# Optimization experiments

Hardware: AMD Instinct MI355X
Metric: run time of the kernel (lower is better)

The kernel has to match this reference:

```python
import jax, jax.numpy as jnp
import numpy as np


def setup_inputs() -> dict:
    key = jax.random.key(0)
    ks = jax.random.split(key, 13)
    HID = 256
    N = 2 * HID                      # hidden_dim * 2
    B_DOC, S, T_K = 32, 40, 64      # docs, sentences/doc, max words/sentence
    B_SENT = B_DOC * S               # total sentences = sum(sent_lens)
    MAX_DOC_LEN = S * T_K
    f = jnp.float32
    sc = jnp.float32(0.05)
    sent_lens = jnp.full((B_DOC,), S, dtype=jnp.int32)
    inp = {
        "s_t_hat": jax.random.normal(ks[0], (B_DOC, N), f),
        "encoder_outputs": jax.random.normal(ks[1], (B_SENT, T_K, N), f),
        "encoder_feature": jax.random.normal(ks[2], (B_SENT * T_K, N), f) * jnp.float32(0.5),
        "seq_lens2": jax.random.randint(ks[3], (B_SENT,), T_K // 2, T_K + 1, dtype=jnp.int32),
        "sent_s_t_hat": jax.random.normal(ks[4], (B_DOC, N), f),
        "sent_enc_outputs": jax.random.normal(ks[5], (B_DOC, S, N), f),
        "sent_enc_feature": jax.random.normal(ks[6], (B_DOC * S, N), f) * jnp.float32(0.5),
        "sent_enc_padding_mask": (jnp.arange(S)[None, :] < sent_lens[:, None]).astype(f),
        "sent_lens": sent_lens,
        "max_doc_len": MAX_DOC_LEN,
        "coverage": jnp.zeros((B_SENT, T_K), f),
        "Wd": jax.random.normal(ks[7], (N, N), f) * sc,
        "bd": jax.random.normal(ks[8], (N,), f) * sc,
        "v_w": jax.random.normal(ks[9], (N,), f) * sc,
        "Wsd": jax.random.normal(ks[10], (N, N), f) * sc,
        "bsd": jax.random.normal(ks[11], (N,), f) * sc,
        "sv_w": jax.random.normal(ks[12], (N,), f) * sc,
    }
    return inp


def _excl_cumsum(x):
    return jnp.cumsum(x) - x


def reference(s_t_hat, encoder_outputs, encoder_feature, seq_lens2, sent_s_t_hat,
              sent_enc_outputs, sent_enc_feature, sent_enc_padding_mask, sent_lens,
              max_doc_len, coverage, Wd, bd, v_w, Wsd, bsd, sv_w):
    B_SENT, T_K, N = encoder_outputs.shape
    B_DOC, S, _ = sent_enc_outputs.shape
    dtype = encoder_outputs.dtype

    # sentence s -> owning doc (replaces first Python loop: broadcast dec_fea per doc)
    doc_ids = jnp.repeat(jnp.arange(B_DOC), sent_lens, total_repeat_length=B_SENT)

    # ---- word-level additive attention over each sentence ----
    dec_fea = s_t_hat @ Wd + bd                              # [B_DOC, N]
    att = jnp.tanh(encoder_feature.reshape(B_SENT, T_K, N) + dec_fea[doc_ids][:, None, :])
    scores = att @ v_w                                        # [B_SENT, T_K]
    w_mask = (jnp.arange(T_K)[None, :] < seq_lens2[:, None]).astype(dtype)
    w_attn_ = jax.nn.softmax(scores, axis=1) * w_mask
    w_attn = w_attn_ / w_attn_.sum(1, keepdims=True)          # [B_SENT, T_K]

    # ---- sentence-level additive attention over each doc ----
    sent_dec_fea = sent_s_t_hat @ Wsd + bsd                   # [B_DOC, N]
    sent_att = jnp.tanh(sent_enc_feature.reshape(B_DOC, S, N) + sent_dec_fea[:, None, :])
    sent_scores = sent_att @ sv_w                             # [B_DOC, S]
    sent_attn_ = jax.nn.softmax(sent_scores, axis=1) * sent_enc_padding_mask
    sent_attn_dist = sent_attn_ / sent_attn_.sum(1, keepdims=True)

    # ---- ragged flatten: scatter valid words of each sentence into its doc stream ----
    sent_start = _excl_cumsum(sent_lens)                      # first sentence idx per doc
    sent_local = jnp.arange(B_SENT) - sent_start[doc_ids]     # sentence pos within doc
    mult_attn = sent_attn_dist[doc_ids, sent_local][:, None] * w_attn  # [B_SENT, T_K]

    word_cum = _excl_cumsum(seq_lens2)                        # global word offsets
    doc_word_off = word_cum - word_cum[sent_start[doc_ids]]   # offset within doc
    pos = doc_word_off[:, None] + jnp.arange(T_K)[None, :]    # [B_SENT, T_K]
    valid = jnp.arange(T_K)[None, :] < seq_lens2[:, None]
    flat = jnp.where(valid, doc_ids[:, None] * max_doc_len + pos, B_DOC * max_doc_len)
    flat = flat.reshape(-1)

    enc_output2 = (jnp.zeros((B_DOC * max_doc_len, N), dtype)
                   .at[flat].set(encoder_outputs.reshape(-1, N), mode="drop")
                   .reshape(B_DOC, max_doc_len, N))
    attn_dist_sw = (jnp.zeros((B_DOC * max_doc_len,), dtype)
                    .at[flat].set(mult_attn.reshape(-1), mode="drop")
                    .reshape(B_DOC, max_doc_len))

    c_t = jnp.einsum("bl,bln->bn", attn_dist_sw, enc_output2)  # [B_DOC, N]
    return (c_t, attn_dist_sw, coverage, sent_attn_dist)
```

## Files before the change

### kernel.cpp

```cpp
#include <hip/hip_runtime.h>
#include <hip/hip_bf16.h>
#include <math.h>

#define B_DOC 32
#define S_MAX 40
#define T_K 64
#define N_DIM 512
#define B_SENT (B_DOC * S_MAX)
#define MAXDOC (S_MAX * T_K)
#define KCHUNK 4

__device__ __forceinline__ float fast_tanh(float x) {
    float e = __expf(2.0f * x);
    return 1.0f - 2.0f * __builtin_amdgcn_rcpf(e + 1.0f);
}

__global__ __launch_bounds__(256) void prep_kernel(
        const int* __restrict__ seq_lens2, const int* __restrict__ sent_lens,
        int* __restrict__ doc_ids, int* __restrict__ sent_local,
        int* __restrict__ doc_word_off, int* __restrict__ sent_start_g,
        int* __restrict__ doc_words_total) {
    __shared__ int ss[B_DOC + 1];
    __shared__ int wc[B_SENT + 1];
    __shared__ int wsum[4];
    int tid = threadIdx.x;
    int lane = tid & 63, w = tid >> 6;

    int ls[5];
    #pragma unroll
    for (int k = 0; k < 5; ++k) ls[k] = seq_lens2[tid * 5 + k];
    int sum = ls[0] + ls[1] + ls[2] + ls[3] + ls[4];

    int scan = sum;
    #pragma unroll
    for (int off = 1; off < 64; off <<= 1) {
        int v = __shfl_up(scan, off, 64);
        if (lane >= off) scan += v;
    }
    if (lane == 63) wsum[w] = scan;

    if (w == 0) {
        int sl = (lane < B_DOC) ? sent_lens[lane] : 0;
        int sc2 = sl;
        #pragma unroll
        for (int off = 1; off < 64; off <<= 1) {
            int v = __shfl_up(sc2, off, 64);
            if (lane >= off) sc2 += v;
        }
        if (lane < B_DOC) ss[lane + 1] = sc2;
        if (lane == 0) ss[0] = 0;
    }
    __syncthreads();

    int wbase = 0;
    for (int i = 0; i < w; ++i) wbase += wsum[i];
    int excl = wbase + scan - sum;
    #pragma unroll
    for (int k = 0; k < 5; ++k) { wc[tid * 5 + k] = excl; excl += ls[k]; }
    if (tid == 255) wc[B_SENT] = excl;
    __syncthreads();

    if (tid <= B_DOC) sent_start_g[tid] = ss[tid];
    if (tid < B_DOC) doc_words_total[tid] = wc[ss[tid + 1]] - wc[ss[tid]];

    for (int i = tid; i < B_SENT; i += 256) {
        int lo = 0, hi = B_DOC - 1;
        while (lo < hi) { int mid = (lo + hi + 1) >> 1; if (ss[mid] <= i) lo = mid; else hi = mid - 1; }
        doc_ids[i] = lo;
        sent_local[i] = i - ss[lo];
        doc_word_off[i] = wc[i] - wc[ss[lo]];
    }
}

__global__ __launch_bounds__(256) void fea_kernel(
        const float* __restrict__ s_t_hat, const float* __restrict__ sent_s_t_hat,
        const float* __restrict__ Wd, const float* __restrict__ bd,
        const float* __restrict__ Wsd, const float* __restrict__ bsd,
        float* __restrict__ fea_part) {
    int blk = blockIdx.x;
    int c = blk & (KCHUNK - 1);
    int b = (blk >> 2) & 31;
    int m = blk >> 7;
    const int KC = N_DIM / KCHUNK;
    const float* x = (m ? sent_s_t_hat : s_t_hat) + b * N_DIM + c * KC;
    const float* W = (m ? Wsd : Wd) + (size_t)c * KC * N_DIM;
    const float* bias = (m ? bsd : bd);
    float* out = fea_part + ((size_t)(m * 32 + b) * KCHUNK + c) * N_DIM;
    __shared__ float xs[128];
    int tid = threadIdx.x;
    if (tid < KC) xs[tid] = x[tid];
    __syncthreads();
    float a0 = 0.f, a1 = 0.f;
    if (c == 0) { a0 = bias[tid]; a1 = bias[tid + 256]; }
    #pragma unroll 8
    for (int k = 0; k < KC; ++k) {
        float xv = xs[k];
        a0 = fmaf(xv, W[k * N_DIM + tid], a0);
        a1 = fmaf(xv, W[k * N_DIM + tid + 256], a1);
    }
    out[tid] = a0;
    out[tid + 256] = a1;
}

__global__ __launch_bounds__(256) void sent_attn_kernel(
        const float* __restrict__ sef, const float* __restrict__ fea_part,
        const float* __restrict__ sv_w, const float* __restrict__ mask,
        float* __restrict__ out_sent) {
    int b = blockIdx.x;
    __shared__ float df[N_DIM];
    __shared__ float vw[N_DIM];
    __shared__ float sc[S_MAX];
    int tid = threadIdx.x;
    const float* fp = fea_part + (size_t)(32 + b) * KCHUNK * N_DIM;
    for (int i = tid; i < N_DIM; i += 256) {
        df[i] = fp[i] + fp[N_DIM + i] + fp[2 * N_DIM + i] + fp[3 * N_DIM + i];
        vw[i] = sv_w[i];
    }
    __syncthreads();
    int w = tid >> 6, lane = tid & 63;
    const float4* sef4 = (const float4*)(sef + (size_t)b * S_MAX * N_DIM);
    const float4* df4 = (const float4*)df;
    const float4* vw4 = (const float4*)vw;
    for (int t = w; t < S_MAX; t += 4) {
        float acc = 0.0f;
        #pragma unroll
        for (int j = 0; j < 2; ++j) {
            int n4 = lane + 64 * j;
            float4 e = sef4[t * 128 + n4];
            float4 d = df4[n4];
            float4 v = vw4[n4];
            acc = fmaf(v.x, fast_tanh(e.x + d.x), acc);
            acc = fmaf(v.y, fast_tanh(e.y + d.y), acc);
            acc = fmaf(v.z, fast_tanh(e.z + d.z), acc);
            acc = fmaf(v.w, fast_tanh(e.w + d.w), acc);
        }
        #pragma unroll
        for (int off = 32; off >= 1; off >>= 1) acc += __shfl_xor(acc, off, 64);
        if (lane == 0) sc[t] = acc;
    }
    __syncthreads();
    if (tid < 64) {
        bool valid = tid < S_MAX;
        float x = valid ? sc[tid] : -INFINITY;
        float m = x;
        #pragma unroll
        for (int off = 32; off >= 1; off >>= 1) m = fmaxf(m, __shfl_xor(m, off, 64));
        float mk = valid ? mask[b * S_MAX + tid] : 0.0f;
        float e = valid ? __expf(x - m) * mk : 0.0f;
        float ssum = e;
        #pragma unroll
        for (int off = 32; off >= 1; off >>= 1) ssum += __shfl_xor(ssum, off, 64);
        if (valid) out_sent[b * S_MAX + tid] = e / ssum;
    }
}

__global__ __launch_bounds__(256) void fused_kernel(
        const float* __restrict__ ef, const float* __restrict__ eo,
        const float* __restrict__ fea_part, const float* __restrict__ v_w,
        const float* __restrict__ sent_attn, const int* __restrict__ seq_lens2,
        const int* __restrict__ doc_ids, const int* __restrict__ sent_local,
        const int* __restrict__ doc_word_off, const int* __restrict__ sent_start,
        const int* __restrict__ doc_words_total, const int* __restrict__ mdl,
        const float* __restrict__ cov_in,
        float* __restrict__ part, float* __restrict__ out_attn,
        float* __restrict__ out_cov) {
    int s = blockIdx.x;
    int tid = threadIdx.x;
    __shared__ float df[N_DIM];
    __shared__ float vw[N_DIM];
    __shared__ float sc[T_K];
    __shared__ float mult[T_K];
    __shared__ float4 red[256];

    int doc = doc_ids[s];
    int len = seq_lens2[s];
    int maxdoc = mdl[0];

    const float* fp = fea_part + (size_t)doc * KCHUNK * N_DIM;
    for (int i = tid; i < N_DIM; i += 256) {
        df[i] = fp[i] + fp[N_DIM + i] + fp[2 * N_DIM + i] + fp[3 * N_DIM + i];
        vw[i] = v_w[i];
    }
    if (tid < T_K) out_cov[s * T_K + tid] = cov_in[s * T_K + tid];
    __syncthreads();

    int w = tid >> 6, lane = tid & 63;
    const float4* ef4 = (const float4*)(ef + (size_t)s * T_K * N_DIM);
    const float4* df4 = (const float4*)df;
    const float4* vw4 = (const float4*)vw;
    for (int t = w; t < len; t += 4) {
        float acc = 0.0f;
        #pragma unroll
        for (int j = 0; j < 2; ++j) {
            int n4 = lane + 64 * j;
            float4 e = ef4[t * 128 + n4];
            float4 d = df4[n4];
            float4 v = vw4[n4];
            acc = fmaf(v.x, fast_tanh(e.x + d.x), acc);
            acc = fmaf(v.y, fast_tanh(e.y + d.y), acc);
            acc = fmaf(v.z, fast_tanh(e.z + d.z), acc);
            acc = fmaf(v.w, fast_tanh(e.w + d.w), acc);
        }
        #pragma unroll
        for (int off = 32; off >= 1; off >>= 1) acc += __shfl_xor(acc, off, 64);
        if (lane == 0) sc[t] = acc;
    }
    __syncthreads();
    if (tid < T_K) {
        bool valid = tid < len;
        float x = valid ? sc[tid] : -INFINITY;
        float m = x;
        #pragma unroll
        for (int off = 32; off >= 1; off >>= 1) m = fmaxf(m, __shfl_xor(m, off, 64));
        float e = valid ? __expf(x - m) : 0.0f;
        float ssum = e;
        #pragma unroll
        for (int off = 32; off >= 1; off >>= 1) ssum += __shfl_xor(ssum, off, 64);
        float sa = sent_attn[doc * S_MAX + sent_local[s]];
        float mu = valid ? sa * (e / ssum) : 0.0f;
        mult[tid] = mu;
        if (valid) out_attn[(size_t)doc * maxdoc + doc_word_off[s] + tid] = mu;
    }
    if (s + 1 == sent_start[doc + 1]) {
        int dwt = doc_words_total[doc];
        for (int i = dwt + tid; i < maxdoc; i += 256)
            out_attn[(size_t)doc * maxdoc + i] = 0.0f;
    }
    __syncthreads();

    int nq = tid & 127;
    int tq = tid >> 7;
    float4 acc = {0.f, 0.f, 0.f, 0.f};
    const float4* e4 = (const float4*)(eo + (size_t)s * T_K * N_DIM);
    for (int t = tq; t < len; t += 2) {
        float m = mult[t];
        float4 e = e4[t * 128 + nq];
        acc.x = fmaf(m, e.x, acc.x);
        acc.y = fmaf(m, e.y, acc.y);
        acc.z = fmaf(m, e.z, acc.z);
        acc.w = fmaf(m, e.w, acc.w);
    }
    red[tid] = acc;
    __syncthreads();
    if (tq == 0) {
        float4 a = red[nq];
        float4 o = red[nq + 128];
        float4 r = {a.x + o.x, a.y + o.y, a.z + o.z, a.w + o.w};
        ((float4*)(part + (size_t)s * N_DIM))[nq] = r;
    }
}

__global__ __launch_bounds__(128) void reduce_kernel(
        const float* __restrict__ part, const int* __restrict__ sent_start,
        float* __restrict__ c_t) {
    int b = blockIdx.x;
    int nq = threadIdx.x;
    int st = sent_start[b], en = sent_start[b + 1];
    float4 acc = {0.f, 0.f, 0.f, 0.f};
    for (int s = st; s < en; ++s) {
        float4 p = ((const float4*)(part + (size_t)s * N_DIM))[nq];
        acc.x += p.x; acc.y += p.y; acc.z += p.z; acc.w += p.w;
    }
    ((float4*)(c_t + (size_t)b * N_DIM))[nq] = acc;
}

extern "C" void kernel_launch(void* const* d_in, const int* in_sizes, int n_in,
                              void* d_out, int out_size, void* d_ws, size_t ws_size,
                              hipStream_t stream) {
    const float* s_t_hat        = (const float*)d_in[0];
    const float* encoder_out    = (const float*)d_in[1];
    const float* encoder_feat   = (const float*)d_in[2];
    const int*   seq_lens2      = (const int*)d_in[3];
    const float* sent_s_t_hat   = (const float*)d_in[4];
    const float* sent_enc_feat  = (const float*)d_in[6];
    const float* sent_pad_mask  = (const float*)d_in[7];
    const int*   sent_lens      = (const int*)d_in[8];
    const int*   max_doc_len    = (const int*)d_in[9];
    const float* coverage       = (const float*)d_in[10];
    const float* Wd             = (const float*)d_in[11];
    const float* bd             = (const float*)d_in[12];
    const float* v_w            = (const float*)d_in[13];
    const float* Wsd            = (const float*)d_in[14];
    const float* bsd            = (const float*)d_in[15];
    const float* sv_w           = (const float*)d_in[16];

    float* out      = (float*)d_out;
    float* o_ct     = out;
    float* o_attn   = out + B_DOC * N_DIM;
    float* o_cov    = o_attn + B_DOC * MAXDOC;
    float* o_sent   = o_cov + B_SENT * T_K;

    float* ws          = (float*)d_ws;
    float* fea_part    = ws;
    float* part        = ws + 131072;
    int*   ints        = (int*)(ws + 131072 + 655360);
    int*   doc_ids     = ints;
    int*   sent_local  = ints + B_SENT;
    int*   doc_w_off   = ints + 2 * B_SENT;
    int*   sent_start  = ints + 3 * B_SENT;
    int*   doc_wtot    = ints + 3 * B_SENT + 33;

    prep_kernel<<<1, 256, 0, stream>>>(seq_lens2, sent_lens, doc_ids, sent_local,
                                       doc_w_off, sent_start, doc_wtot);
    fea_kernel<<<2 * 32 * KCHUNK, 256, 0, stream>>>(s_t_hat, sent_s_t_hat, Wd, bd,
                                                    Wsd, bsd, fea_part);
    sent_attn_kernel<<<B_DOC, 256, 0, stream>>>(sent_enc_feat, fea_part, sv_w,
                                                sent_pad_mask, o_sent);
    fused_kernel<<<B_SENT, 256, 0, stream>>>(encoder_feat, encoder_out, fea_part,
                                             v_w, o_sent, seq_lens2, doc_ids,
                                             sent_local, doc_w_off, sent_start,
                                             doc_wtot, max_doc_len, coverage,
                                             part, o_attn, o_cov);
    reduce_kernel<<<B_DOC, 128, 0, stream>>>(part, sent_start, o_ct);
}
```

Measured before the change: 80.51 us.

## Fuse word attention with context accumulation via online softmax; merge prep and fea kernels

The word-level scoring and the weighted sum over encoder outputs now run in a single pass. Each wavefront keeps a running max, a running sum and a rescaled accumulator, and the four wavefronts are merged at the end. This removes the separate softmax phase, the extra barriers and the second loop over encoder_outputs, and it prefetches the next encoder_feature row. The prep and feature-projection kernels are merged into one launch, with one extra block handling the scans, which saves a kernel launch. The cost is more registers and extra exp/rescale work per step.

```diff
diff --git a/kernel.cpp b/kernel.cpp
--- a/kernel.cpp
+++ b/kernel.cpp
@@ -15,91 +15,90 @@
     return 1.0f - 2.0f * __builtin_amdgcn_rcpf(e + 1.0f);
 }
 
-__global__ __launch_bounds__(256) void prep_kernel(
+__global__ __launch_bounds__(256) void prep_fea_kernel(
         const int* __restrict__ seq_lens2, const int* __restrict__ sent_lens,
+        const float* __restrict__ s_t_hat, const float* __restrict__ sent_s_t_hat,
+        const float* __restrict__ Wd, const float* __restrict__ bd,
+        const float* __restrict__ Wsd, const float* __restrict__ bsd,
+        float* __restrict__ fea_part,
         int* __restrict__ doc_ids, int* __restrict__ sent_local,
         int* __restrict__ doc_word_off, int* __restrict__ sent_start_g,
         int* __restrict__ doc_words_total) {
-    __shared__ int ss[B_DOC + 1];
-    __shared__ int wc[B_SENT + 1];
-    __shared__ int wsum[4];
     int tid = threadIdx.x;
-    int lane = tid & 63, w = tid >> 6;
-
-    int ls[5];
-    #pragma unroll
-    for (int k = 0; k < 5; ++k) ls[k] = seq_lens2[tid * 5 + k];
-    int sum = ls[0] + ls[1] + ls[2] + ls[3] + ls[4];
-
-    int scan = sum;
-    #pragma unroll
-    for (int off = 1; off < 64; off <<= 1) {
-        int v = __shfl_up(scan, off, 64);
-        if (lane >= off) scan += v;
-    }
-    if (lane == 63) wsum[w] = scan;
-
-    if (w == 0) {
-        int sl = (lane < B_DOC) ? sent_lens[lane] : 0;
-        int sc2 = sl;
+    if (blockIdx.x == 256) {
+        __shared__ int ss[B_DOC + 1];
+        __shared__ int wc[B_SENT + 1];
+        __shared__ int wsum[4];
+        int lane = tid & 63, w = tid >> 6;
+
+        int ls[5];
+        #pragma unroll
+        for (int k = 0; k < 5; ++k) ls[k] = seq_lens2[tid * 5 + k];
+        int sum = ls[0] + ls[1] + ls[2] + ls[3] + ls[4];
+
+        int scan = sum;
         #pragma unroll
         for (int off = 1; off < 64; off <<= 1) {
-            int v = __shfl_up(sc2, off, 64);
-            if (lane >= off) sc2 += v;
-        }
-        if (lane < B_DOC) ss[lane + 1] = sc2;
-        if (lane == 0) ss[0] = 0;
-    }
-    __syncthreads();
-
-    int wbase = 0;
-    for (int i = 0; i < w; ++i) wbase += wsum[i];
-    int excl = wbase + scan - sum;
-    #pragma unroll
-    for (int k = 0; k < 5; ++k) { wc[tid * 5 + k] = excl; excl += ls[k]; }
-    if (tid == 255) wc[B_SENT] = excl;
-    __syncthreads();
-
-    if (tid <= B_DOC) sent_start_g[tid] = ss[tid];
-    if (tid < B_DOC) doc_words_total[tid] = wc[ss[tid + 1]] - wc[ss[tid]];
-
-    for (int i = tid; i < B_SENT; i += 256) {
-        int lo = 0, hi = B_DOC - 1;
-        while (lo < hi) { int mid = (lo + hi + 1) >> 1; if (ss[mid] <= i) lo = mid; else hi = mid - 1; }
-        doc_ids[i] = lo;
-        sent_local[i] = i - ss[lo];
-        doc_word_off[i] = wc[i] - wc[ss[lo]];
-    }
-}
-
-__global__ __launch_bounds__(256) void fea_kernel(
-        const float* __restrict__ s_t_hat, const float* __restrict__ sent_s_t_hat,
-        const float* __restrict__ Wd, const float* __restrict__ bd,
-        const float* __restrict__ Wsd, const float* __restrict__ bsd,
-        float* __restrict__ fea_part) {
-    int blk = blockIdx.x;
-    int c = blk & (KCHUNK - 1);
-    int b = (blk >> 2) & 31;
-    int m = blk >> 7;
-    const int KC = N_DIM / KCHUNK;
-    const float* x = (m ? sent_s_t_hat : s_t_hat) + b * N_DIM + c * KC;
-    const float* W = (m ? Wsd : Wd) + (size_t)c * KC * N_DIM;
-    const float* bias = (m ? bsd : bd);
-    float* out = fea_part + ((size_t)(m * 32 + b) * KCHUNK + c) * N_DIM;
-    __shared__ float xs[128];
-    int tid = threadIdx.x;
-    if (tid < KC) xs[tid] = x[tid];
-    __syncthreads();
-    float a0 = 0.f, a1 = 0.f;
-    if (c == 0) { a0 = bias[tid]; a1 = bias[tid + 256]; }
-    #pragma unroll 8
-    for (int k = 0; k < KC; ++k) {
-        float xv = xs[k];
-        a0 = fmaf(xv, W[k * N_DIM + tid], a0);
-        a1 = fmaf(xv, W[k * N_DIM + tid + 256], a1);
-    }
-    out[tid] = a0;
-    out[tid + 256] = a1;
+            int v = __shfl_up(scan, off, 64);
+            if (lane >= off) scan += v;
+        }
+        if (lane == 63) wsum[w] = scan;
+
+        if (w == 0) {
+            int sl = (lane < B_DOC) ? sent_lens[lane] : 0;
+            int sc2 = sl;
+            #pragma unroll
+            for (int off = 1; off < 64; off <<= 1) {
+                int v = __shfl_up(sc2, off, 64);
+                if (lane >= off) sc2 += v;
+            }
+            if (lane < B_DOC) ss[lane + 1] = sc2;
+            if (lane == 0) ss[0] = 0;
+        }
+        __syncthreads();
+
+        int wbase = 0;
+        for (int i = 0; i < w; ++i) wbase += wsum[i];
+        int excl = wbase + scan - sum;
+        #pragma unroll
+        for (int k = 0; k < 5; ++k) { wc[tid * 5 + k] = excl; excl += ls[k]; }
+        if (tid == 255) wc[B_SENT] = excl;
+        __syncthreads();
+
+        if (tid <= B_DOC) sent_start_g[tid] = ss[tid];
+        if (tid < B_DOC) doc_words_total[tid] = wc[ss[tid + 1]] - wc[ss[tid]];
+
+        for (int i = tid; i < B_SENT; i += 256) {
+            int lo = 0, hi = B_DOC - 1;
+            while (lo < hi) { int mid = (lo + hi + 1) >> 1; if (ss[mid] <= i) lo = mid; else hi = mid - 1; }
+            doc_ids[i] = lo;
+            sent_local[i] = i - ss[lo];
+            doc_word_off[i] = wc[i] - wc[ss[lo]];
+        }
+    } else {
+        int blk = blockIdx.x;
+        int c = blk & (KCHUNK - 1);
+        int b = (blk >> 2) & 31;
+        int m = blk >> 7;
+        const int KC = N_DIM / KCHUNK;
+        const float* x = (m ? sent_s_t_hat : s_t_hat) + b * N_DIM + c * KC;
+        const float* W = (m ? Wsd : Wd) + (size_t)c * KC * N_DIM;
+        const float* bias = (m ? bsd : bd);
+        float* out = fea_part + ((size_t)(m * 32 + b) * KCHUNK + c) * N_DIM;
+        __shared__ float xs[128];
+        if (tid < KC) xs[tid] = x[tid];
+        __syncthreads();
+        float a0 = 0.f, a1 = 0.f;
+        if (c == 0) { a0 = bias[tid]; a1 = bias[tid + 256]; }
+        #pragma unroll 8
+        for (int k = 0; k < KC; ++k) {
+            float xv = xs[k];
+            a0 = fmaf(xv, W[k * N_DIM + tid], a0);
+            a1 = fmaf(xv, W[k * N_DIM + tid + 256], a1);
+        }
+        out[tid] = a0;
+        out[tid + 256] = a1;
+    }
 }
 
 __global__ __launch_bounds__(256) void sent_attn_kernel(
@@ -154,7 +153,7 @@
     }
 }
 
-__global__ __launch_bounds__(256) void fused_kernel(
+__global__ __launch_bounds__(256, 4) void fused_kernel(
         const float* __restrict__ ef, const float* __restrict__ eo,
         const float* __restrict__ fea_part, const float* __restrict__ v_w,
         const float* __restrict__ sent_attn, const int* __restrict__ seq_lens2,
@@ -166,87 +165,97 @@
         float* __restrict__ out_cov) {
     int s = blockIdx.x;
     int tid = threadIdx.x;
-    __shared__ float df[N_DIM];
-    __shared__ float vw[N_DIM];
+    int w = tid >> 6, lane = tid & 63;
     __shared__ float sc[T_K];
-    __shared__ float mult[T_K];
-    __shared__ float4 red[256];
+    __shared__ float wm[4], wl[4];
+    __shared__ float4 red[4][128];
 
     int doc = doc_ids[s];
     int len = seq_lens2[s];
     int maxdoc = mdl[0];
 
-    const float* fp = fea_part + (size_t)doc * KCHUNK * N_DIM;
-    for (int i = tid; i < N_DIM; i += 256) {
-        df[i] = fp[i] + fp[N_DIM + i] + fp[2 * N_DIM + i] + fp[3 * N_DIM + i];
-        vw[i] = v_w[i];
-    }
+    const float4* fp4 = (const float4*)(fea_part + (size_t)doc * KCHUNK * N_DIM);
+    float4 d0 = fp4[lane], d1 = fp4[64 + lane];
+    #pragma unroll
+    for (int c = 1; c < KCHUNK; ++c) {
+        float4 a = fp4[c * 128 + lane], b = fp4[c * 128 + 64 + lane];
+        d0.x += a.x; d0.y += a.y; d0.z += a.z; d0.w += a.w;
+        d1.x += b.x; d1.y += b.y; d1.z += b.z; d1.w += b.w;
+    }
+    const float4* vw4 = (const float4*)v_w;
+    float4 v0 = vw4[lane], v1 = vw4[64 + lane];
+
     if (tid < T_K) out_cov[s * T_K + tid] = cov_in[s * T_K + tid];
-    __syncthreads();
-
-    int w = tid >> 6, lane = tid & 63;
+
     const float4* ef4 = (const float4*)(ef + (size_t)s * T_K * N_DIM);
-    const float4* df4 = (const float4*)df;
-    const float4* vw4 = (const float4*)vw;
+    const float4* eo4 = (const float4*)(eo + (size_t)s * T_K * N_DIM);
+
+    float m_w = -INFINITY, l_w = 0.0f;
+    float4 O0 = {0.f, 0.f, 0.f, 0.f}, O1 = {0.f, 0.f, 0.f, 0.f};
+
+    float4 ea0, ea1;
+    if (w < len) { ea0 = ef4[w * 128 + lane]; ea1 = ef4[w * 128 + 64 + lane]; }
     for (int t = w; t < len; t += 4) {
-        float acc = 0.0f;
-        #pragma unroll
-        for (int j = 0; j < 2; ++j) {
-            int n4 = lane + 64 * j;
-            float4 e = ef4[t * 128 + n4];
-            float4 d = df4[n4];
-            float4 v = vw4[n4];
-            acc = fmaf(v.x, fast_tanh(e.x + d.x), acc);
-            acc = fmaf(v.y, fast_tanh(e.y + d.y), acc);
-            acc = fmaf(v.z, fast_tanh(e.z + d.z), acc);
-            acc = fmaf(v.w, fast_tanh(e.w + d.w), acc);
-        }
+        float4 p0 = eo4[t * 128 + lane];
+        float4 p1 = eo4[t * 128 + 64 + lane];
+        float4 eb0, eb1;
+        int tn = t + 4;
+        if (tn < len) { eb0 = ef4[tn * 128 + lane]; eb1 = ef4[tn * 128 + 64 + lane]; }
+        float acc;
+        acc  = v0.x * fast_tanh(ea0.x + d0.x);
+        acc = fmaf(v0.y, fast_tanh(ea0.y + d0.y), acc);
+        acc = fmaf(v0.z, fast_tanh(ea0.z + d0.z), acc);
+        acc = fmaf(v0.w, fast_tanh(ea0.w + d0.w), acc);
+        acc = fmaf(v1.x, fast_tanh(ea1.x + d1.x), acc);
+        acc = fmaf(v1.y, fast_tanh(ea1.y + d1.y), acc);
+        acc = fmaf(v1.z, fast_tanh(ea1.z + d1.z), acc);
+        acc = fmaf(v1.w, fast_tanh(ea1.w + d1.w), acc);
         #pragma unroll
         for (int off = 32; off >= 1; off >>= 1) acc += __shfl_xor(acc, off, 64);
         if (lane == 0) sc[t] = acc;
-    }
+        if (acc > m_w) {
+            float r = __expf(m_w - acc);
+            l_w *= r;
+            O0.x *= r; O0.y *= r; O0.z *= r; O0.w *= r;
+            O1.x *= r; O1.y *= r; O1.z *= r; O1.w *= r;
+            m_w = acc;
+        }
+        float p = __expf(acc - m_w);
+        l_w += p;
+        O0.x = fmaf(p, p0.x, O0.x); O0.y = fmaf(p, p0.y, O0.y);
+        O0.z = fmaf(p, p0.z, O0.z); O0.w = fmaf(p, p0.w, O0.w);
+        O1.x = fmaf(p, p1.x, O1.x); O1.y = fmaf(p, p1.y, O1.y);
+        O1.z = fmaf(p, p1.z, O1.z); O1.w = fmaf(p, p1.w, O1.w);
+        ea0 = eb0; ea1 = eb1;
+    }
+
+    if (lane == 0) { wm[w] = m_w; wl[w] = l_w; }
     __syncthreads();
-    if (tid < T_K) {
-        bool valid = tid < len;
-        float x = valid ? sc[tid] : -INFINITY;
-        float m = x;
-        #pragma unroll
-        for (int off = 32; off >= 1; off >>= 1) m = fmaxf(m, __shfl_xor(m, off, 64));
-        float e = valid ? __expf(x - m) : 0.0f;
-        float ssum = e;
-        #pragma unroll
-        for (int off = 32; off >= 1; off >>= 1) ssum += __shfl_xor(ssum, off, 64);
-        float sa = sent_attn[doc * S_MAX + sent_local[s]];
-        float mu = valid ? sa * (e / ssum) : 0.0f;
-        mult[tid] = mu;
-        if (valid) out_attn[(size_t)doc * maxdoc + doc_word_off[s] + tid] = mu;
+    float m = fmaxf(fmaxf(wm[0], wm[1]), fmaxf(wm[2], wm[3]));
+    float l = __expf(wm[0] - m) * wl[0] + __expf(wm[1] - m) * wl[1]
+            + __expf(wm[2] - m) * wl[2] + __expf(wm[3] - m) * wl[3];
+    float fw = __expf(m_w - m);
+    red[w][lane].x = O0.x * fw; red[w][lane].y = O0.y * fw;
+    red[w][lane].z = O0.z * fw; red[w][lane].w = O0.w * fw;
+    red[w][64 + lane].x = O1.x * fw; red[w][64 + lane].y = O1.y * fw;
+    red[w][64 + lane].z = O1.z * fw; red[w][64 + lane].w = O1.w * fw;
+    float sa = sent_attn[doc * S_MAX + sent_local[s]];
+    float inv = sa / l;
+    __syncthreads();
+    if (tid < 128) {
+        float4 a = red[0][tid], b = red[1][tid], c = red[2][tid], d = red[3][tid];
+        float4 r = {(a.x + b.x + c.x + d.x) * inv, (a.y + b.y + c.y + d.y) * inv,
+                    (a.z + b.z + c.z + d.z) * inv, (a.w + b.w + c.w + d.w) * inv};
+        ((float4*)(part + (size_t)s * N_DIM))[tid] = r;
+    }
+    if (tid < T_K && tid < len) {
+        float mu = sa * __expf(sc[tid] - m) / l;
+        out_attn[(size_t)doc * maxdoc + doc_word_off[s] + tid] = mu;
     }
     if (s + 1 == sent_start[doc + 1]) {
         int dwt = doc_words_total[doc];
         for (int i = dwt + tid; i < maxdoc; i += 256)
             out_attn[(size_t)doc * maxdoc + i] = 0.0f;
-    }
-    __syncthreads();
-
-    int nq = tid & 127;
-    int tq = tid >> 7;
-    float4 acc = {0.f, 0.f, 0.f, 0.f};
-    const float4* e4 = (const float4*)(eo + (size_t)s * T_K * N_DIM);
-    for (int t = tq; t < len; t += 2) {
-        float m = mult[t];
-        float4 e = e4[t * 128 + nq];
-        acc.x = fmaf(m, e.x, acc.x);
-        acc.y = fmaf(m, e.y, acc.y);
-        acc.z = fmaf(m, e.z, acc.z);
-        acc.w = fmaf(m, e.w, acc.w);
-    }
-    red[tid] = acc;
-    __syncthreads();
-    if (tq == 0) {
-        float4 a = red[nq];
-        float4 o = red[nq + 128];
-        float4 r = {a.x + o.x, a.y + o.y, a.z + o.z, a.w + o.w};
-        ((float4*)(part + (size_t)s * N_DIM))[nq] = r;
     }
 }
 
@@ -300,10 +309,10 @@
     int*   sent_start  = ints + 3 * B_SENT;
     int*   doc_wtot    = ints + 3 * B_SENT + 33;
 
-    prep_kernel<<<1, 256, 0, stream>>>(seq_lens2, sent_lens, doc_ids, sent_local,
-                                       doc_w_off, sent_start, doc_wtot);
-    fea_kernel<<<2 * 32 * KCHUNK, 256, 0, stream>>>(s_t_hat, sent_s_t_hat, Wd, bd,
-                                                    Wsd, bsd, fea_part);
+    prep_fea_kernel<<<257, 256, 0, stream>>>(seq_lens2, sent_lens, s_t_hat,
+                                             sent_s_t_hat, Wd, bd, Wsd, bsd,
+                                             fea_part, doc_ids, sent_local,
+                                             doc_w_off, sent_start, doc_wtot);
     sent_attn_kernel<<<B_DOC, 256, 0, stream>>>(sent_enc_feat, fea_part, sv_w,
                                                 sent_pad_mask, o_sent);
     fused_kernel<<<B_SENT, 256, 0, stream>>>(encoder_feat, encoder_out, fea_part,
```

Measured after the change: 77.47 us. 1.04x faster.

## Split fused attention into finer-grained score, softmax and context kernels

Applied to the files above, without the earlier changes.

Merges the prep scan and feature GEMV into a single launch, using an extra block for the scan. The old per-sentence fused kernel is split into a word-score kernel (8 rows per block), a sentence-score kernel, a softmax/mult kernel with one wave per sentence that also computes the sentence softmax, and a context kernel that splits each sentence into two halves. The goal is more parallelism and better latency hiding for the memory-bound passes over encoder features and outputs. The cost is two extra launches, more global round trips for scores and weights, and twice as many partial context rows to reduce.

```diff
diff --git a/kernel.cpp b/kernel.cpp
--- a/kernel.cpp
+++ b/kernel.cpp
@@ -15,239 +15,235 @@
     return 1.0f - 2.0f * __builtin_amdgcn_rcpf(e + 1.0f);
 }
 
-__global__ __launch_bounds__(256) void prep_kernel(
+__global__ __launch_bounds__(256) void prep_fea_kernel(
         const int* __restrict__ seq_lens2, const int* __restrict__ sent_lens,
+        const float* __restrict__ s_t_hat, const float* __restrict__ sent_s_t_hat,
+        const float* __restrict__ Wd, const float* __restrict__ bd,
+        const float* __restrict__ Wsd, const float* __restrict__ bsd,
+        float* __restrict__ fea_part,
         int* __restrict__ doc_ids, int* __restrict__ sent_local,
         int* __restrict__ doc_word_off, int* __restrict__ sent_start_g,
         int* __restrict__ doc_words_total) {
-    __shared__ int ss[B_DOC + 1];
-    __shared__ int wc[B_SENT + 1];
-    __shared__ int wsum[4];
     int tid = threadIdx.x;
-    int lane = tid & 63, w = tid >> 6;
-
-    int ls[5];
-    #pragma unroll
-    for (int k = 0; k < 5; ++k) ls[k] = seq_lens2[tid * 5 + k];
-    int sum = ls[0] + ls[1] + ls[2] + ls[3] + ls[4];
-
-    int scan = sum;
-    #pragma unroll
-    for (int off = 1; off < 64; off <<= 1) {
-        int v = __shfl_up(scan, off, 64);
-        if (lane >= off) scan += v;
-    }
-    if (lane == 63) wsum[w] = scan;
-
-    if (w == 0) {
-        int sl = (lane < B_DOC) ? sent_lens[lane] : 0;
-        int sc2 = sl;
+    if (blockIdx.x == 256) {
+        __shared__ int ss[B_DOC + 1];
+        __shared__ int wc[B_SENT + 1];
+        __shared__ int wsum[4];
+        int lane = tid & 63, w = tid >> 6;
+
+        int ls[5];
+        #pragma unroll
+        for (int k = 0; k < 5; ++k) ls[k] = seq_lens2[tid * 5 + k];
+        int sum = ls[0] + ls[1] + ls[2] + ls[3] + ls[4];
+
+        int scan = sum;
         #pragma unroll
         for (int off = 1; off < 64; off <<= 1) {
-            int v = __shfl_up(sc2, off, 64);
-            if (lane >= off) sc2 += v;
-        }
-        if (lane < B_DOC) ss[lane + 1] = sc2;
-        if (lane == 0) ss[0] = 0;
+            int v = __shfl_up(scan, off, 64);
+            if (lane >= off) scan += v;
+        }
+        if (lane == 63) wsum[w] = scan;
+
+        if (w == 0) {
+            int sl = (lane < B_DOC) ? sent_lens[lane] : 0;
+            int sc2 = sl;
+            #pragma unroll
+            for (int off = 1; off < 64; off <<= 1) {
+                int v = __shfl_up(sc2, off, 64);
+                if (lane >= off) sc2 += v;
+            }
+            if (lane < B_DOC) ss[lane + 1] = sc2;
+            if (lane == 0) ss[0] = 0;
+        }
+        __syncthreads();
+
+        int wbase = 0;
+        for (int i = 0; i < w; ++i) wbase += wsum[i];
+        int excl = wbase + scan - sum;
+        #pragma unroll
+        for (int k = 0; k < 5; ++k) { wc[tid * 5 + k] = excl; excl += ls[k]; }
+        if (tid == 255) wc[B_SENT] = excl;
+        __syncthreads();
+
+        if (tid <= B_DOC) sent_start_g[tid] = ss[tid];
+        if (tid < B_DOC) doc_words_total[tid] = wc[ss[tid + 1]] - wc[ss[tid]];
+
+        for (int i = tid; i < B_SENT; i += 256) {
+            int lo = 0, hi = B_DOC - 1;
+            while (lo < hi) { int mid = (lo + hi + 1) >> 1; if (ss[mid] <= i) lo = mid; else hi = mid - 1; }
+            doc_ids[i] = lo;
+            sent_local[i] = i - ss[lo];
+            doc_word_off[i] = wc[i] - wc[ss[lo]];
+        }
+    } else {
+        int blk = blockIdx.x;
+        int c = blk & (KCHUNK - 1);
+        int b = (blk >> 2) & 31;
+        int m = blk >> 7;
+        const int KC = N_DIM / KCHUNK;
+        const float* x = (m ? sent_s_t_hat : s_t_hat) + b * N_DIM + c * KC;
+        const float* W = (m ? Wsd : Wd) + (size_t)c * KC * N_DIM;
+        const float* bias = (m ? bsd : bd);
+        float* out = fea_part + ((size_t)(m * 32 + b) * KCHUNK + c) * N_DIM;
+        __shared__ float xs[128];
+        if (tid < KC) xs[tid] = x[tid];
+        __syncthreads();
+        float a0 = 0.f, a1 = 0.f;
+        if (c == 0) { a0 = bias[tid]; a1 = bias[tid + 256]; }
+        #pragma unroll 8
+        for (int k = 0; k < KC; ++k) {
+            float xv = xs[k];
+            a0 = fmaf(xv, W[k * N_DIM + tid], a0);
+            a1 = fmaf(xv, W[k * N_DIM + tid + 256], a1);
+        }
+        out[tid] = a0;
+        out[tid + 256] = a1;
+    }
+}
+
+__device__ __forceinline__ void score_tile(
+        const float4* __restrict__ src,
+        const float* __restrict__ fp,
+        const float* __restrict__ vwg,
+        int nrows,
+        float* __restrict__ out_sc) {
+    __shared__ __align__(16) float tile[8 * N_DIM];
+    __shared__ __align__(16) float dfs[N_DIM];
+    __shared__ __align__(16) float vws[N_DIM];
+    int tid = threadIdx.x;
+    float4* t4 = (float4*)tile;
+    #pragma unroll
+    for (int j = 0; j < 4; ++j) t4[j * 256 + tid] = src[j * 256 + tid];
+    for (int i = tid; i < N_DIM; i += 256) {
+        dfs[i] = fp[i] + fp[N_DIM + i] + fp[2 * N_DIM + i] + fp[3 * N_DIM + i];
+        vws[i] = vwg[i];
     }
     __syncthreads();
-
-    int wbase = 0;
-    for (int i = 0; i < w; ++i) wbase += wsum[i];
-    int excl = wbase + scan - sum;
-    #pragma unroll
-    for (int k = 0; k < 5; ++k) { wc[tid * 5 + k] = excl; excl += ls[k]; }
-    if (tid == 255) wc[B_SENT] = excl;
-    __syncthreads();
-
-    if (tid <= B_DOC) sent_start_g[tid] = ss[tid];
-    if (tid < B_DOC) doc_words_total[tid] = wc[ss[tid + 1]] - wc[ss[tid]];
-
-    for (int i = tid; i < B_SENT; i += 256) {
-        int lo = 0, hi = B_DOC - 1;
-        while (lo < hi) { int mid = (lo + hi + 1) >> 1; if (ss[mid] <= i) lo = mid; else hi = mid - 1; }
-        doc_ids[i] = lo;
-        sent_local[i] = i - ss[lo];
-        doc_word_off[i] = wc[i] - wc[ss[lo]];
-    }
-}
-
-__global__ __launch_bounds__(256) void fea_kernel(
-        const float* __restrict__ s_t_hat, const float* __restrict__ sent_s_t_hat,
-        const float* __restrict__ Wd, const float* __restrict__ bd,
-        const float* __restrict__ Wsd, const float* __restrict__ bsd,
-        float* __restrict__ fea_part) {
-    int blk = blockIdx.x;
-    int c = blk & (KCHUNK - 1);
-    int b = (blk >> 2) & 31;
-    int m = blk >> 7;
-    const int KC = N_DIM / KCHUNK;
-    const float* x = (m ? sent_s_t_hat : s_t_hat) + b * N_DIM + c * KC;
-    const float* W = (m ? Wsd : Wd) + (size_t)c * KC * N_DIM;
-    const float* bias = (m ? bsd : bd);
-    float* out = fea_part + ((size_t)(m * 32 + b) * KCHUNK + c) * N_DIM;
-    __shared__ float xs[128];
-    int tid = threadIdx.x;
-    if (tid < KC) xs[tid] = x[tid];
-    __syncthreads();
-    float a0 = 0.f, a1 = 0.f;
-    if (c == 0) { a0 = bias[tid]; a1 = bias[tid + 256]; }
-    #pragma unroll 8
-    for (int k = 0; k < KC; ++k) {
-        float xv = xs[k];
-        a0 = fmaf(xv, W[k * N_DIM + tid], a0);
-        a1 = fmaf(xv, W[k * N_DIM + tid + 256], a1);
-    }
-    out[tid] = a0;
-    out[tid + 256] = a1;
-}
-
-__global__ __launch_bounds__(256) void sent_attn_kernel(
+    int g = tid >> 5, sub = tid & 31;
+    float acc = 0.0f;
+    const float4* row = t4 + g * 128;
+    const float4* d4 = (const float4*)dfs;
+    const float4* v4 = (const float4*)vws;
+    #pragma unroll
+    for (int k = 0; k < 4; ++k) {
+        int j = sub + k * 32;
+        float4 e = row[j];
+        float4 d = d4[j];
+        float4 v = v4[j];
+        acc = fmaf(v.x, fast_tanh(e.x + d.x), acc);
+        acc = fmaf(v.y, fast_tanh(e.y + d.y), acc);
+        acc = fmaf(v.z, fast_tanh(e.z + d.z), acc);
+        acc = fmaf(v.w, fast_tanh(e.w + d.w), acc);
+    }
+    #pragma unroll
+    for (int off = 16; off >= 1; off >>= 1) acc += __shfl_xor(acc, off, 32);
+    if (sub == 0 && g < nrows) out_sc[g] = acc;
+}
+
+__global__ __launch_bounds__(256) void word_score_kernel(
+        const float* __restrict__ ef, const float* __restrict__ fea_part,
+        const float* __restrict__ v_w, const int* __restrict__ seq_lens2,
+        const int* __restrict__ doc_ids, float* __restrict__ w_sc) {
+    int s = blockIdx.x >> 3, c = blockIdx.x & 7;
+    int len = seq_lens2[s];
+    if (c * 8 >= len) return;
+    int doc = doc_ids[s];
+    const float4* src = (const float4*)ef + ((size_t)s * T_K + c * 8) * 128;
+    score_tile(src, fea_part + (size_t)doc * KCHUNK * N_DIM, v_w,
+               min(8, len - c * 8), w_sc + s * T_K + c * 8);
+}
+
+__global__ __launch_bounds__(256) void sent_score_kernel(
         const float* __restrict__ sef, const float* __restrict__ fea_part,
-        const float* __restrict__ sv_w, const float* __restrict__ mask,
-        float* __restrict__ out_sent) {
-    int b = blockIdx.x;
-    __shared__ float df[N_DIM];
-    __shared__ float vw[N_DIM];
-    __shared__ float sc[S_MAX];
-    int tid = threadIdx.x;
-    const float* fp = fea_part + (size_t)(32 + b) * KCHUNK * N_DIM;
-    for (int i = tid; i < N_DIM; i += 256) {
-        df[i] = fp[i] + fp[N_DIM + i] + fp[2 * N_DIM + i] + fp[3 * N_DIM + i];
-        vw[i] = sv_w[i];
-    }
-    __syncthreads();
-    int w = tid >> 6, lane = tid & 63;
-    const float4* sef4 = (const float4*)(sef + (size_t)b * S_MAX * N_DIM);
-    const float4* df4 = (const float4*)df;
-    const float4* vw4 = (const float4*)vw;
-    for (int t = w; t < S_MAX; t += 4) {
-        float acc = 0.0f;
-        #pragma unroll
-        for (int j = 0; j < 2; ++j) {
-            int n4 = lane + 64 * j;
-            float4 e = sef4[t * 128 + n4];
-            float4 d = df4[n4];
-            float4 v = vw4[n4];
-            acc = fmaf(v.x, fast_tanh(e.x + d.x), acc);
-            acc = fmaf(v.y, fast_tanh(e.y + d.y), acc);
-            acc = fmaf(v.z, fast_tanh(e.z + d.z), acc);
-            acc = fmaf(v.w, fast_tanh(e.w + d.w), acc);
-        }
-        #pragma unroll
-        for (int off = 32; off >= 1; off >>= 1) acc += __shfl_xor(acc, off, 64);
-        if (lane == 0) sc[t] = acc;
-    }
-    __syncthreads();
-    if (tid < 64) {
-        bool valid = tid < S_MAX;
-        float x = valid ? sc[tid] : -INFINITY;
-        float m = x;
-        #pragma unroll
-        for (int off = 32; off >= 1; off >>= 1) m = fmaxf(m, __shfl_xor(m, off, 64));
-        float mk = valid ? mask[b * S_MAX + tid] : 0.0f;
-        float e = valid ? __expf(x - m) * mk : 0.0f;
-        float ssum = e;
-        #pragma unroll
-        for (int off = 32; off >= 1; off >>= 1) ssum += __shfl_xor(ssum, off, 64);
-        if (valid) out_sent[b * S_MAX + tid] = e / ssum;
-    }
-}
-
-__global__ __launch_bounds__(256) void fused_kernel(
-        const float* __restrict__ ef, const float* __restrict__ eo,
-        const float* __restrict__ fea_part, const float* __restrict__ v_w,
-        const float* __restrict__ sent_attn, const int* __restrict__ seq_lens2,
+        const float* __restrict__ sv_w, float* __restrict__ sent_sc) {
+    int doc = blockIdx.x / 5, c = blockIdx.x % 5;
+    const float4* src = (const float4*)sef + ((size_t)doc * S_MAX + c * 8) * 128;
+    score_tile(src, fea_part + (size_t)(32 + doc) * KCHUNK * N_DIM, sv_w,
+               8, sent_sc + doc * S_MAX + c * 8);
+}
+
+__global__ __launch_bounds__(256) void softmax_mult_kernel(
+        const float* __restrict__ w_sc, const float* __restrict__ sent_sc,
+        const float* __restrict__ mask, const int* __restrict__ seq_lens2,
         const int* __restrict__ doc_ids, const int* __restrict__ sent_local,
         const int* __restrict__ doc_word_off, const int* __restrict__ sent_start,
         const int* __restrict__ doc_words_total, const int* __restrict__ mdl,
         const float* __restrict__ cov_in,
-        float* __restrict__ part, float* __restrict__ out_attn,
-        float* __restrict__ out_cov) {
-    int s = blockIdx.x;
+        float* __restrict__ w_mult, float* __restrict__ out_attn,
+        float* __restrict__ out_cov, float* __restrict__ o_sent) {
     int tid = threadIdx.x;
-    __shared__ float df[N_DIM];
-    __shared__ float vw[N_DIM];
-    __shared__ float sc[T_K];
-    __shared__ float mult[T_K];
-    __shared__ float4 red[256];
-
+    int w = tid >> 6, lane = tid & 63;
+    int s = blockIdx.x * 4 + w;
     int doc = doc_ids[s];
+    int local = sent_local[s];
     int len = seq_lens2[s];
     int maxdoc = mdl[0];
 
-    const float* fp = fea_part + (size_t)doc * KCHUNK * N_DIM;
-    for (int i = tid; i < N_DIM; i += 256) {
-        df[i] = fp[i] + fp[N_DIM + i] + fp[2 * N_DIM + i] + fp[3 * N_DIM + i];
-        vw[i] = v_w[i];
-    }
-    if (tid < T_K) out_cov[s * T_K + tid] = cov_in[s * T_K + tid];
-    __syncthreads();
-
-    int w = tid >> 6, lane = tid & 63;
-    const float4* ef4 = (const float4*)(ef + (size_t)s * T_K * N_DIM);
-    const float4* df4 = (const float4*)df;
-    const float4* vw4 = (const float4*)vw;
-    for (int t = w; t < len; t += 4) {
-        float acc = 0.0f;
-        #pragma unroll
-        for (int j = 0; j < 2; ++j) {
-            int n4 = lane + 64 * j;
-            float4 e = ef4[t * 128 + n4];
-            float4 d = df4[n4];
-            float4 v = vw4[n4];
-            acc = fmaf(v.x, fast_tanh(e.x + d.x), acc);
-            acc = fmaf(v.y, fast_tanh(e.y + d.y), acc);
-            acc = fmaf(v.z, fast_tanh(e.z + d.z), acc);
-            acc = fmaf(v.w, fast_tanh(e.w + d.w), acc);
-        }
-        #pragma unroll
-        for (int off = 32; off >= 1; off >>= 1) acc += __shfl_xor(acc, off, 64);
-        if (lane == 0) sc[t] = acc;
-    }
-    __syncthreads();
-    if (tid < T_K) {
-        bool valid = tid < len;
-        float x = valid ? sc[tid] : -INFINITY;
-        float m = x;
-        #pragma unroll
-        for (int off = 32; off >= 1; off >>= 1) m = fmaxf(m, __shfl_xor(m, off, 64));
-        float e = valid ? __expf(x - m) : 0.0f;
-        float ssum = e;
-        #pragma unroll
-        for (int off = 32; off >= 1; off >>= 1) ssum += __shfl_xor(ssum, off, 64);
-        float sa = sent_attn[doc * S_MAX + sent_local[s]];
-        float mu = valid ? sa * (e / ssum) : 0.0f;
-        mult[tid] = mu;
-        if (valid) out_attn[(size_t)doc * maxdoc + doc_word_off[s] + tid] = mu;
+    int gi = blockIdx.x * 256 + tid;
+    out_cov[gi] = cov_in[gi];
+
+    float sx = (lane < S_MAX) ? sent_sc[doc * S_MAX + lane] : -INFINITY;
+    float sm = sx;
+    #pragma unroll
+    for (int off = 32; off >= 1; off >>= 1) sm = fmaxf(sm, __shfl_xor(sm, off, 64));
+    float se = (lane < S_MAX) ? __expf(sx - sm) : 0.0f;
+    float ssum = se;
+    #pragma unroll
+    for (int off = 32; off >= 1; off >>= 1) ssum += __shfl_xor(ssum, off, 64);
+    float mk = (lane < S_MAX) ? mask[doc * S_MAX + lane] : 0.0f;
+    float sem = se * mk;
+    float ssum2 = sem;
+    #pragma unroll
+    for (int off = 32; off >= 1; off >>= 1) ssum2 += __shfl_xor(ssum2, off, 64);
+    float sdist = sem / ssum2;
+    if (local == 0 && lane < S_MAX) o_sent[doc * S_MAX + lane] = sdist;
+    float sa = __shfl(sdist, local, 64);
+
+    float x = (lane < len) ? w_sc[s * T_K + lane] : -INFINITY;
+    float m = x;
+    #pragma unroll
+    for (int off = 32; off >= 1; off >>= 1) m = fmaxf(m, __shfl_xor(m, off, 64));
+    float e = (lane < len) ? __expf(x - m) : 0.0f;
+    float l = e;
+    #pragma unroll
+    for (int off = 32; off >= 1; off >>= 1) l += __shfl_xor(l, off, 64);
+    float mu = sa * e / l;
+    if (lane < len) {
+        w_mult[s * T_K + lane] = mu;
+        out_attn[(size_t)doc * maxdoc + doc_word_off[s] + lane] = mu;
     }
     if (s + 1 == sent_start[doc + 1]) {
         int dwt = doc_words_total[doc];
-        for (int i = dwt + tid; i < maxdoc; i += 256)
+        for (int i = dwt + lane; i < maxdoc; i += 64)
             out_attn[(size_t)doc * maxdoc + i] = 0.0f;
     }
-    __syncthreads();
-
-    int nq = tid & 127;
-    int tq = tid >> 7;
+}
+
+__global__ __launch_bounds__(128) void context_kernel(
+        const float* __restrict__ eo, const float* __restrict__ w_mult,
+        const int* __restrict__ seq_lens2, float* __restrict__ part) {
+    int s = blockIdx.x >> 1, h = blockIdx.x & 1;
+    int tid = threadIdx.x;
+    int len = seq_lens2[s];
+    int t0 = h * 32;
+    __shared__ float lm[32];
     float4 acc = {0.f, 0.f, 0.f, 0.f};
-    const float4* e4 = (const float4*)(eo + (size_t)s * T_K * N_DIM);
-    for (int t = tq; t < len; t += 2) {
-        float m = mult[t];
-        float4 e = e4[t * 128 + nq];
-        acc.x = fmaf(m, e.x, acc.x);
-        acc.y = fmaf(m, e.y, acc.y);
-        acc.z = fmaf(m, e.z, acc.z);
-        acc.w = fmaf(m, e.w, acc.w);
-    }
-    red[tid] = acc;
-    __syncthreads();
-    if (tq == 0) {
-        float4 a = red[nq];
-        float4 o = red[nq + 128];
-        float4 r = {a.x + o.x, a.y + o.y, a.z + o.z, a.w + o.w};
-        ((float4*)(part + (size_t)s * N_DIM))[nq] = r;
-    }
+    if (t0 < len) {
+        int te = min(len, t0 + 32);
+        if (tid < 32) lm[tid] = (t0 + tid < te) ? w_mult[s * T_K + t0 + tid] : 0.0f;
+        __syncthreads();
+        const float4* e4 = (const float4*)eo + ((size_t)s * T_K + t0) * 128;
+        #pragma unroll 8
+        for (int t = 0; t < te - t0; ++t) {
+            float m = lm[t];
+            float4 e = e4[t * 128 + tid];
+            acc.x = fmaf(m, e.x, acc.x);
+            acc.y = fmaf(m, e.y, acc.y);
+            acc.z = fmaf(m, e.z, acc.z);
+            acc.w = fmaf(m, e.w, acc.w);
+        }
+    }
+    ((float4*)(part + (size_t)blockIdx.x * N_DIM))[tid] = acc;
 }
 
 __global__ __launch_bounds__(128) void reduce_kernel(
@@ -257,8 +253,8 @@
     int nq = threadIdx.x;
     int st = sent_start[b], en = sent_start[b + 1];
     float4 acc = {0.f, 0.f, 0.f, 0.f};
-    for (int s = st; s < en; ++s) {
-        float4 p = ((const float4*)(part + (size_t)s * N_DIM))[nq];
+    for (int r = 2 * st; r < 2 * en; ++r) {
+        float4 p = ((const float4*)(part + (size_t)r * N_DIM))[nq];
         acc.x += p.x; acc.y += p.y; acc.z += p.z; acc.w += p.w;
     }
     ((float4*)(c_t + (size_t)b * N_DIM))[nq] = acc;
@@ -293,23 +289,30 @@
     float* ws          = (float*)d_ws;
     float* fea_part    = ws;
     float* part        = ws + 131072;
-    int*   ints        = (int*)(ws + 131072 + 655360);
+    float* w_sc        = ws + 131072 + 1310720;
+    float* w_mult      = w_sc + 81920;
+    float* sent_sc     = w_mult + 81920;
+    int*   ints        = (int*)(sent_sc + 1280);
     int*   doc_ids     = ints;
     int*   sent_local  = ints + B_SENT;
     int*   doc_w_off   = ints + 2 * B_SENT;
     int*   sent_start  = ints + 3 * B_SENT;
     int*   doc_wtot    = ints + 3 * B_SENT + 33;
 
-    prep_kernel<<<1, 256, 0, stream>>>(seq_lens2, sent_lens, doc_ids, sent_local,
-                                       doc_w_off, sent_start, doc_wtot);
-    fea_kernel<<<2 * 32 * KCHUNK, 256, 0, stream>>>(s_t_hat, sent_s_t_hat, Wd, bd,
-                                                    Wsd, bsd, fea_part);
-    sent_attn_kernel<<<B_DOC, 256, 0, stream>>>(sent_enc_feat, fea_part, sv_w,
-                                                sent_pad_mask, o_sent);
-    fused_kernel<<<B_SENT, 256, 0, stream>>>(encoder_feat, encoder_out, fea_part,
-                                             v_w, o_sent, seq_lens2, doc_ids,
-                                             sent_local, doc_w_off, sent_start,
-                                             doc_wtot, max_doc_len, coverage,
-                                             part, o_attn, o_cov);
+    prep_fea_kernel<<<257, 256, 0, stream>>>(seq_lens2, sent_lens, s_t_hat,
+                                             sent_s_t_hat, Wd, bd, Wsd, bsd,
+                                             fea_part, doc_ids, sent_local,
+                                             doc_w_off, sent_start, doc_wtot);
+    word_score_kernel<<<B_SENT * 8, 256, 0, stream>>>(encoder_feat, fea_part, v_w,
+                                                      seq_lens2, doc_ids, w_sc);
+    sent_score_kernel<<<B_DOC * 5, 256, 0, stream>>>(sent_enc_feat, fea_part,
+                                                     sv_w, sent_sc);
+    softmax_mult_kernel<<<320, 256, 0, stream>>>(w_sc, sent_sc, sent_pad_mask,
+                                                 seq_lens2, doc_ids, sent_local,
+                                                 doc_w_off, sent_start, doc_wtot,
+                                                 max_doc_len, coverage,
+                                                 w_mult, o_attn, o_cov, o_sent);
+    context_kernel<<<B_SENT * 2, 128, 0, stream>>>(encoder_out, w_mult,
+                                                   seq_lens2, part);
     reduce_kernel<<<B_DOC, 128, 0, stream>>>(part, sent_start, o_ct);
 }
```

Result: slower. 89.46 us (+11.1%).
